# Optimization experiments

Hardware: AMD Instinct MI355X
Metric: run time of the kernel (lower is better)

The kernel has to match this reference:

```python
import jax, jax.numpy as jnp
import numpy as np

B, C, H, W, NH = 1, 192, 448, 448, 6
D = C // NH  # head dim = 32


def setup_inputs() -> dict:
    key = jax.random.key(0)
    ks = jax.random.split(key, 6)
    s = 0.02  # weight init scale
    return {
        "x": jax.random.normal(ks[0], (B, C, H, W), jnp.float32),
        "condition": jax.random.uniform(ks[1], (B, C, H, W), jnp.float32),
        "ln_g": jnp.ones((C,), jnp.float32),
        "ln_b": jnp.zeros((C,), jnp.float32),
        "pre_w": jax.random.normal(ks[2], (C, C), jnp.float32) * s,   # 1x1 conv [out,in]
        "pre_b": jnp.zeros((C,), jnp.float32),
        "qkv_w": jax.random.normal(ks[3], (3 * C, C), jnp.float32) * s,
        "mn_w": jax.random.normal(ks[4], (2 * D, D), jnp.float32) * s,  # Linear(d, 2d), [out,in]
        "gating": jnp.ones((1, 2 * NH, 1, 1), jnp.float32),
        "proj_w": jax.random.normal(ks[5], (C, C), jnp.float32) * s,
    }


def _gsa(x, condition, ln_g, ln_b, pre_w, pre_b, qkv_w, mn_w, gating, proj_w):
    b, c, h, w = x.shape
    nh = NH
    d = c // nh
    hw = h * w
    # ConvenientLayerNorm: LayerNorm over the channel axis per pixel (biased var, eps=1e-5)
    mu = jnp.mean(x, axis=1, keepdims=True)
    var = jnp.var(x, axis=1, keepdims=True)
    xn = (x - mu) * jax.lax.rsqrt(var + 1e-5)
    xn = xn * ln_g[None, :, None, None] + ln_b[None, :, None, None]
    # 1x1 convs == channel matmuls
    y = jnp.einsum('bchw,oc->bohw', xn, pre_w) + pre_b[None, :, None, None]
    qkv = jnp.einsum('bchw,oc->bohw', y, qkv_w)
    q, k, v = jnp.split(qkv, 3, axis=1)
    rs = lambda t: t.reshape(b, nh, d, hw)
    q, k, v = rs(q), rs(k), rs(v)
    # F.normalize over spatial axis (eps=1e-12)
    l2 = lambda t: t / jnp.maximum(jnp.linalg.norm(t, axis=-1, keepdims=True), 1e-12)
    q, k = l2(q), l2(k)
    # channel-wise attention scores [b,nh,d,d]
    attn = jnp.einsum('bhds,bhes->bhde', q, k)
    # mn_conv: Linear(d -> 2d) on last axis, then chunk
    mn = jnp.einsum('bhde,ge->bhdg', attn, mn_w)  # [b,nh,d,2d]
    m, n = jnp.split(mn, 2, axis=-1)
    g1, g2 = jnp.split(gating, 2, axis=1)  # each [1,nh,1,1]
    gm = g1 * m + g2 * n  # g1*(m@illu)+g2*(n@illu) == (g1*m+g2*n)@illu (per-head scalars)
    illu = condition.reshape(b, nh, d, hw)
    mi = jnp.einsum('bhde,bhes->bhds', gm, illu)  # [b,nh,d,hw]
    out = jax.nn.softmax(mi * v, axis=-2)  # softmax over head-dim axis d
    out = out.reshape(b, c, h, w)
    out = jnp.einsum('bchw,oc->bohw', out, proj_w) + x
    return out


def reference(x, condition, ln_g, ln_b, pre_w, pre_b, qkv_w, mn_w, gating, proj_w):
    return _gsa(x, condition, ln_g, ln_b, pre_w, pre_b, qkv_w, mn_w, gating, proj_w)
```

## Files before the change

### kernel.cpp

```cpp
#include <hip/hip_runtime.h>

typedef short s8v __attribute__((ext_vector_type(8)));
typedef short s4v __attribute__((ext_vector_type(4)));
typedef float f4v __attribute__((ext_vector_type(4)));

#define HW     200704
#define NCH    192
#define PT     64
#define CMP    68
#define PMP    200
#define GRID   512
#define NTILES 3136

__device__ __forceinline__ float b2f(unsigned short u){
    unsigned int i = ((unsigned int)u) << 16; float f;
    __builtin_memcpy(&f, &i, 4); return f;
}
__device__ __forceinline__ unsigned short f2b(float f){
    unsigned int i; __builtin_memcpy(&i, &f, 4);
    i += 0x7FFFu + ((i >> 16) & 1u);
    return (unsigned short)(i >> 16);
}
__device__ __forceinline__ int swz(int oct, int p){
    return (oct & ~7) | ((oct + 2*(p & 7)) & 7);
}

__global__ void gsa_prep(const float* __restrict__ pre_w, const float* __restrict__ qkv_w,
                         const float* __restrict__ proj_w, unsigned short* __restrict__ wbf,
                         float* __restrict__ accs, unsigned int* __restrict__ ctr)
{
    int i = blockIdx.x*256 + threadIdx.x;
    if (i < 2)      ctr[i] = 0u;
    if (i < 6528)   accs[i] = 0.f;
    if (i < 36864)  wbf[i]           = f2b(pre_w[i]);
    if (i < 110592) wbf[36864 + i]   = f2b(qkv_w[i]);
    if (i < 36864)  wbf[147456 + i]  = f2b(proj_w[i]);
}

__global__ __launch_bounds__(384, 3) void gsa_k1(
    const float* __restrict__ x,
    const float* __restrict__ lng,
    const float* __restrict__ lnb,
    const unsigned short* __restrict__ pre_wb,
    const float* __restrict__ pre_b,
    const unsigned short* __restrict__ qkv_wb,
    unsigned short* __restrict__ v_out,
    float* __restrict__ gram_red,
    float* __restrict__ sq_red,
    unsigned int* __restrict__ ctr)
{
    __shared__ __align__(16) unsigned char smem[26112*2 + 25600 + 1536];
    __shared__ int t_sh;
    unsigned short* bufA  = (unsigned short*)smem;
    unsigned short* bufP1 = (unsigned short*)(smem + 26112);
    unsigned short* bufP2 = (unsigned short*)(smem + 2*26112);
    float* sq_lds = (float*)(smem + 2*26112 + 25600);
    float* stats  = (float*)bufP2;

    const int tid  = threadIdx.x;
    const int wid  = tid >> 6;
    const int lane = tid & 63;
    const int l15  = lane & 15;
    const int quad = lane >> 4;

    f4v gacc[4];
    #pragma unroll
    for (int g = 0; g < 4; ++g) gacc[g] = (f4v){0.f, 0.f, 0.f, 0.f};
    sq_lds[tid] = 0.f;

    auto gemm2 = [&](int co, f4v (&acc)[2][4]) {
        #pragma unroll
        for (int j = 0; j < 2; ++j)
            #pragma unroll
            for (int nt = 0; nt < 4; ++nt) acc[j][nt] = (f4v){0.f,0.f,0.f,0.f};
        #pragma unroll
        for (int ks = 0; ks < 6; ++ks) {
            s8v a[2];
            #pragma unroll
            for (int j = 0; j < 2; ++j)
                a[j] = *(const s8v*)(qkv_wb + (size_t)(co*NCH + wid*32 + j*16 + l15)*NCH + ks*32 + quad*8);
            #pragma unroll
            for (int nt = 0; nt < 4; ++nt) {
                int p = nt*16 + l15;
                s8v b = *(const s8v*)(bufP2 + p*PMP + swz(ks*4 + quad, p)*8);
                #pragma unroll
                for (int j = 0; j < 2; ++j)
                    acc[j][nt] = __builtin_amdgcn_mfma_f32_16x16x32_bf16(a[j], b, acc[j][nt], 0, 0, 0);
            }
        }
    };

    for (;;) {
        __syncthreads();
        if (tid == 0) t_sh = atomicAdd(ctr, 1u);
        __syncthreads();
        const int t = t_sh;
        if (t >= NTILES) break;
        const int p0 = t * PT;

        {
            const int c0 = tid >> 3, oct = tid & 7;
            #pragma unroll
            for (int pass = 0; pass < 4; ++pass) {
                int c = pass*48 + c0;
                const float* gp = x + (size_t)c*HW + p0 + oct*8;
                f4v f0 = *(const f4v*)(gp);
                f4v f1 = *(const f4v*)(gp + 4);
                s8v w;
                #pragma unroll
                for (int r = 0; r < 4; ++r) { w[r] = (short)f2b(f0[r]); w[4+r] = (short)f2b(f1[r]); }
                *(s8v*)(bufA + c*CMP + oct*8) = w;
            }
        }
        __syncthreads();

        {
            const int p = lane, g = wid;
            float s1 = 0.f, s2 = 0.f;
            #pragma unroll
            for (int i = 0; i < 32; ++i) {
                float v = b2f(bufA[(g*32 + i)*CMP + p]);
                s1 += v; s2 += v*v;
            }
            stats[g*64 + p]       = s1;
            stats[384 + g*64 + p] = s2;
        }
        __syncthreads();
        if (tid < 64) {
            float s1 = 0.f, s2 = 0.f;
            #pragma unroll
            for (int g = 0; g < 6; ++g) { s1 += stats[g*64 + tid]; s2 += stats[384 + g*64 + tid]; }
            float mu  = s1 * (1.f/192.f);
            float var = s2 * (1.f/192.f) - mu*mu;
            stats[768 + tid] = mu;
            stats[832 + tid] = rsqrtf(fmaxf(var, 0.f) + 1e-5f);
        }
        __syncthreads();

        {
            const int p = lane, g = wid;
            const float mu = stats[768 + p], is = stats[832 + p];
            #pragma unroll
            for (int oo = 0; oo < 4; ++oo) {
                s8v w;
                #pragma unroll
                for (int j = 0; j < 8; ++j) {
                    int c = g*32 + oo*8 + j;
                    float v = (b2f(bufA[c*CMP + p]) - mu) * is;
                    v = v * lng[c] + lnb[c];
                    w[j] = (short)f2b(v);
                }
                int oct = g*4 + oo;
                *(s8v*)(bufP1 + p*PMP + swz(oct, p)*8) = w;
            }
        }
        __syncthreads();

        {
            f4v acc[2][4];
            #pragma unroll
            for (int j = 0; j < 2; ++j)
                #pragma unroll
                for (int nt = 0; nt < 4; ++nt) acc[j][nt] = (f4v){0.f,0.f,0.f,0.f};
            #pragma unroll
            for (int ks = 0; ks < 6; ++ks) {
                s8v a[2];
                #pragma unroll
                for (int j = 0; j < 2; ++j)
                    a[j] = *(const s8v*)(pre_wb + (size_t)((wid*2 + j)*16 + l15)*NCH + ks*32 + quad*8);
                #pragma unroll
                for (int nt = 0; nt < 4; ++nt) {
                    int p = nt*16 + l15;
                    s8v b = *(const s8v*)(bufP1 + p*PMP + swz(ks*4 + quad, p)*8);
                    #pragma unroll
                    for (int j = 0; j < 2; ++j)
                        acc[j][nt] = __builtin_amdgcn_mfma_f32_16x16x32_bf16(a[j], b, acc[j][nt], 0, 0, 0);
                }
            }
            #pragma unroll
            for (int j = 0; j < 2; ++j) {
                int c0 = (wid*2 + j)*16 + quad*4;
                f4v pb4 = *(const f4v*)(pre_b + c0);
                int oct = c0 >> 3, half = (c0 >> 2) & 1;
                #pragma unroll
                for (int nt = 0; nt < 4; ++nt) {
                    int p = nt*16 + l15;
                    s4v w;
                    #pragma unroll
                    for (int r = 0; r < 4; ++r)
                        w[r] = (short)f2b(acc[j][nt][r] + pb4[r]);
                    *(s4v*)(bufP2 + p*PMP + swz(oct, p)*8 + half*4) = w;
                }
            }
        }
        __syncthreads();

        {
            f4v acc[2][4];
            gemm2(0, acc);
            #pragma unroll
            for (int j = 0; j < 2; ++j)
                #pragma unroll
                for (int nt = 0; nt < 4; ++nt) {
                    int p = nt*16 + l15;
                    #pragma unroll
                    for (int r = 0; r < 4; ++r) {
                        int c = wid*32 + j*16 + quad*4 + r;
                        bufA[c*CMP + p] = f2b(acc[j][nt][r]);
                    }
                }
            gemm2(1, acc);
            #pragma unroll
            for (int j = 0; j < 2; ++j)
                #pragma unroll
                for (int nt = 0; nt < 4; ++nt) {
                    int p = nt*16 + l15;
                    #pragma unroll
                    for (int r = 0; r < 4; ++r) {
                        int c = wid*32 + j*16 + quad*4 + r;
                        bufP1[c*CMP + p] = f2b(acc[j][nt][r]);
                    }
                }
        }
        __syncthreads();

        {
            const unsigned short* src = (wid < 3) ? (bufA + tid*CMP) : (bufP1 + (tid - 192)*CMP);
            float s = 0.f;
            #pragma unroll
            for (int o = 0; o < 8; ++o) {
                s4v lo = *(const s4v*)(src + o*8);
                s4v hi = *(const s4v*)(src + o*8 + 4);
                #pragma unroll
                for (int e = 0; e < 4; ++e) {
                    float a = b2f((unsigned short)lo[e]);
                    float b = b2f((unsigned short)hi[e]);
                    s += a*a + b*b;
                }
            }
            sq_lds[tid] += s;
        }

        #pragma unroll
        for (int g = 0; g < 4; ++g) {
            int gt = wid*4 + g, h = gt >> 2, dm = (gt >> 1) & 1, em = gt & 1;
            const unsigned short* qrow = bufA  + (h*32 + dm*16 + l15)*CMP;
            const unsigned short* krow = bufP1 + (h*32 + em*16 + l15)*CMP;
            #pragma unroll
            for (int ks = 0; ks < 2; ++ks) {
                int off = ks*32 + quad*8;
                s4v alo = *(const s4v*)(qrow + off), ahi = *(const s4v*)(qrow + off + 4);
                s4v blo = *(const s4v*)(krow + off), bhi = *(const s4v*)(krow + off + 4);
                s8v a = __builtin_shufflevector(alo, ahi, 0,1,2,3,4,5,6,7);
                s8v b = __builtin_shufflevector(blo, bhi, 0,1,2,3,4,5,6,7);
                gacc[g] = __builtin_amdgcn_mfma_f32_16x16x32_bf16(a, b, gacc[g], 0, 0, 0);
            }
        }

        {
            f4v acc[2][4];
            gemm2(2, acc);
            __syncthreads();
            #pragma unroll
            for (int j = 0; j < 2; ++j)
                #pragma unroll
                for (int nt = 0; nt < 4; ++nt) {
                    int p = nt*16 + l15;
                    #pragma unroll
                    for (int r = 0; r < 4; ++r) {
                        int c = wid*32 + j*16 + quad*4 + r;
                        bufA[c*CMP + p] = f2b(acc[j][nt][r]);
                    }
                }
        }
        __syncthreads();
        {
            const int c0 = tid >> 3, oct = tid & 7;
            #pragma unroll
            for (int pass = 0; pass < 4; ++pass) {
                int c = pass*48 + c0;
                s4v lo = *(const s4v*)(bufA + c*CMP + oct*8);
                s4v hi = *(const s4v*)(bufA + c*CMP + oct*8 + 4);
                s8v w = __builtin_shufflevector(lo, hi, 0,1,2,3,4,5,6,7);
                *(s8v*)(v_out + 2*((size_t)c*HW + p0) + oct*8) = w;
            }
        }
    }

    #pragma unroll
    for (int g = 0; g < 4; ++g) {
        int gt = wid*4 + g, h = gt >> 2, dm = (gt >> 1) & 1, em = gt & 1;
        #pragma unroll
        for (int r = 0; r < 4; ++r) {
            int d = dm*16 + quad*4 + r, e = em*16 + l15;
            atomicAdd(&gram_red[h*1024 + d*32 + e], gacc[g][r]);
        }
    }
    atomicAdd(&sq_red[tid], sq_lds[tid]);
}

__global__ void gsa_k2(const float* __restrict__ gram_red, const float* __restrict__ sq_red,
                       const float* __restrict__ mn_w, const float* __restrict__ gating,
                       unsigned short* __restrict__ gm_out)
{
    __shared__ float attn[6144];
    __shared__ float mw[2048];
    __shared__ float inv[384];
    const int tid = threadIdx.x;
    for (int i = tid; i < 384; i += 256)
        inv[i] = 1.f / fmaxf(sqrtf(fmaxf(sq_red[i], 0.f)), 1e-12f);
    for (int i = tid; i < 2048; i += 256) mw[i] = mn_w[i];
    __syncthreads();
    for (int i = tid; i < 6144; i += 256) {
        int h = i >> 10, d = (i >> 5) & 31, e = i & 31;
        attn[i] = gram_red[i] * inv[h*32 + d] * inv[192 + h*32 + e];
    }
    __syncthreads();
    if (tid < 192) {
        int h = tid >> 5, d = tid & 31;
        float g1 = gating[h], g2 = gating[6 + h];
        const float* ar = attn + h*1024 + d*32;
        for (int e = 0; e < 32; ++e) {
            float m = 0.f, n = 0.f;
            for (int c2 = 0; c2 < 32; ++c2) {
                m += ar[c2] * mw[e*32 + c2];
                n += ar[c2] * mw[(e + 32)*32 + c2];
            }
            gm_out[h*1024 + d*32 + e] = f2b(g1*m + g2*n);
        }
    }
}

__global__ __launch_bounds__(384, 3) void gsa_k3(
    const float* __restrict__ cond,
    const float* __restrict__ x,
    const unsigned short* __restrict__ gm,
    const unsigned short* __restrict__ proj_wb,
    const unsigned short* v_in,
    float* out,
    unsigned int* __restrict__ ctr)
{
    __shared__ __align__(16) unsigned char smem[26112 + 25600 + 25600];
    __shared__ int t_sh;
    unsigned short* bufA = (unsigned short*)smem;
    unsigned short* bufB = (unsigned short*)(smem + 26112);
    unsigned short* bufC = (unsigned short*)(smem + 26112 + 25600);

    const int tid  = threadIdx.x;
    const int wid  = tid >> 6;
    const int lane = tid & 63;
    const int l15  = lane & 15;
    const int quad = lane >> 4;

    for (;;) {
        __syncthreads();
        if (tid == 0) t_sh = atomicAdd(ctr + 1, 1u);
        __syncthreads();
        const int t = t_sh;
        if (t >= NTILES) break;
        const int p0 = t * PT;

        {
            const int c0 = tid >> 3, oct = tid & 7;
            #pragma unroll
            for (int pass = 0; pass < 4; ++pass) {
                int c = pass*48 + c0;
                const float* gp = cond + (size_t)c*HW + p0 + oct*8;
                f4v f0 = *(const f4v*)(gp);
                f4v f1 = *(const f4v*)(gp + 4);
                s8v w;
                #pragma unroll
                for (int r = 0; r < 4; ++r) { w[r] = (short)f2b(f0[r]); w[4+r] = (short)f2b(f1[r]); }
                *(s8v*)(bufA + c*CMP + oct*8) = w;
            }
        }
        __syncthreads();
        {
            const int p = lane, g = wid;
            #pragma unroll
            for (int oo = 0; oo < 4; ++oo) {
                int oct = g*4 + oo;
                s8v w;
                #pragma unroll
                for (int j = 0; j < 8; ++j)
                    w[j] = (short)bufA[(oct*8 + j)*CMP + p];
                *(s8v*)(bufB + p*PMP + swz(oct, p)*8) = w;
            }
        }
        __syncthreads();
        {
            const int c0 = tid >> 3, oct = tid & 7;
            #pragma unroll
            for (int pass = 0; pass < 4; ++pass) {
                int c = pass*48 + c0;
                s8v vv = *(const s8v*)(v_in + 2*((size_t)c*HW + p0) + oct*8);
                s4v lo = __builtin_shufflevector(vv, vv, 0,1,2,3);
                s4v hi = __builtin_shufflevector(vv, vv, 4,5,6,7);
                *(s4v*)(bufA + c*CMP + oct*8)     = lo;
                *(s4v*)(bufA + c*CMP + oct*8 + 4) = hi;
            }
        }
        __syncthreads();

        {
            #pragma unroll
            for (int j = 0; j < 4; ++j) {
                int pr = wid*4 + j, h = pr >> 2, nt = pr & 3;
                int p = nt*16 + l15;
                s8v a0 = *(const s8v*)(gm + h*1024 + l15*32 + quad*8);
                s8v a1 = *(const s8v*)(gm + h*1024 + (16 + l15)*32 + quad*8);
                s8v b  = *(const s8v*)(bufB + p*PMP + swz(h*4 + quad, p)*8);
                f4v z = (f4v){0.f,0.f,0.f,0.f};
                f4v m0 = __builtin_amdgcn_mfma_f32_16x16x32_bf16(a0, b, z, 0, 0, 0);
                f4v m1 = __builtin_amdgcn_mfma_f32_16x16x32_bf16(a1, b, z, 0, 0, 0);
                float tv[8];
                #pragma unroll
                for (int r = 0; r < 4; ++r) {
                    tv[r]     = m0[r] * b2f(bufA[(h*32 + quad*4 + r)*CMP + p]);
                    tv[4 + r] = m1[r] * b2f(bufA[(h*32 + 16 + quad*4 + r)*CMP + p]);
                }
                float mx = tv[0];
                #pragma unroll
                for (int r = 1; r < 8; ++r) mx = fmaxf(mx, tv[r]);
                mx = fmaxf(mx, __shfl_xor(mx, 16));
                mx = fmaxf(mx, __shfl_xor(mx, 32));
                float s = 0.f;
                #pragma unroll
                for (int r = 0; r < 8; ++r) { tv[r] = __expf(tv[r] - mx); s += tv[r]; }
                s += __shfl_xor(s, 16);
                s += __shfl_xor(s, 32);
                float is = 1.f / s;
                s4v w0, w1;
                #pragma unroll
                for (int r = 0; r < 4; ++r) {
                    w0[r] = (short)f2b(tv[r] * is);
                    w1[r] = (short)f2b(tv[4 + r] * is);
                }
                int c0 = h*32 + quad*4, c1 = c0 + 16;
                *(s4v*)(bufC + p*PMP + swz(c0 >> 3, p)*8 + ((c0 >> 2) & 1)*4) = w0;
                *(s4v*)(bufC + p*PMP + swz(c1 >> 3, p)*8 + ((c1 >> 2) & 1)*4) = w1;
            }
        }
        __syncthreads();

        {
            f4v acc[2][4];
            #pragma unroll
            for (int j = 0; j < 2; ++j)
                #pragma unroll
                for (int nt = 0; nt < 4; ++nt) acc[j][nt] = (f4v){0.f,0.f,0.f,0.f};
            #pragma unroll
            for (int ks = 0; ks < 6; ++ks) {
                s8v a[2];
                #pragma unroll
                for (int j = 0; j < 2; ++j)
                    a[j] = *(const s8v*)(proj_wb + (size_t)((wid*2 + j)*16 + l15)*NCH + ks*32 + quad*8);
                #pragma unroll
                for (int nt = 0; nt < 4; ++nt) {
                    int p = nt*16 + l15;
                    s8v b = *(const s8v*)(bufC + p*PMP + swz(ks*4 + quad, p)*8);
                    #pragma unroll
                    for (int j = 0; j < 2; ++j)
                        acc[j][nt] = __builtin_amdgcn_mfma_f32_16x16x32_bf16(a[j], b, acc[j][nt], 0, 0, 0);
                }
            }
            __syncthreads();
            #pragma unroll
            for (int j = 0; j < 2; ++j)
                #pragma unroll
                for (int nt = 0; nt < 4; ++nt) {
                    int p = nt*16 + l15;
                    #pragma unroll
                    for (int r = 0; r < 4; ++r) {
                        int c = wid*32 + j*16 + quad*4 + r;
                        bufA[c*CMP + p] = f2b(acc[j][nt][r]);
                    }
                }
        }
        __syncthreads();

        {
            const int c0 = tid >> 3, oct = tid & 7;
            #pragma unroll
            for (int pass = 0; pass < 4; ++pass) {
                int c = pass*48 + c0;
                const float* xp = x + (size_t)c*HW + p0 + oct*8;
                f4v x0 = *(const f4v*)(xp);
                f4v x1 = *(const f4v*)(xp + 4);
                f4v o0, o1;
                #pragma unroll
                for (int r = 0; r < 4; ++r) {
                    o0[r] = b2f(bufA[c*CMP + oct*8 + r])     + x0[r];
                    o1[r] = b2f(bufA[c*CMP + oct*8 + 4 + r]) + x1[r];
                }
                float* op = out + (size_t)c*HW + p0 + oct*8;
                *(f4v*)(op)     = o0;
                *(f4v*)(op + 4) = o1;
            }
        }
    }
}

extern "C" void kernel_launch(void* const* d_in, const int* in_sizes, int n_in,
                              void* d_out, int out_size, void* d_ws, size_t ws_size,
                              hipStream_t stream)
{
    (void)in_sizes; (void)n_in; (void)out_size; (void)ws_size;
    const float* x      = (const float*)d_in[0];
    const float* cond   = (const float*)d_in[1];
    const float* lng    = (const float*)d_in[2];
    const float* lnb    = (const float*)d_in[3];
    const float* pre_w  = (const float*)d_in[4];
    const float* pre_b  = (const float*)d_in[5];
    const float* qkv_w  = (const float*)d_in[6];
    const float* mn_w   = (const float*)d_in[7];
    const float* gating = (const float*)d_in[8];
    const float* proj_w = (const float*)d_in[9];

    char* ws = (char*)d_ws;
    float* gram_red = (float*)ws;
    float* sq_red   = (float*)(ws + 24576);
    unsigned short* gm  = (unsigned short*)(ws + 26112);
    unsigned short* wbf = (unsigned short*)(ws + 38400);
    unsigned int* ctr   = (unsigned int*)(ws + 407040);
    unsigned short* pre_wb  = wbf;
    unsigned short* qkv_wb  = wbf + 36864;
    unsigned short* proj_wb = wbf + 147456;

    gsa_prep<<<432,  256, 0, stream>>>(pre_w, qkv_w, proj_w, wbf, gram_red, ctr);
    gsa_k1 <<<GRID,  384, 0, stream>>>(x, lng, lnb, pre_wb, pre_b, qkv_wb,
                                       (unsigned short*)d_out, gram_red, sq_red, ctr);
    gsa_k2 <<<1,     256, 0, stream>>>(gram_red, sq_red, mn_w, gating, gm);
    gsa_k3 <<<GRID,  384, 0, stream>>>(cond, x, gm, proj_wb,
                                       (const unsigned short*)d_out, (float*)d_out, ctr);
}
```

Baseline: 676.2 us.

## Prefetch next tile into registers and fuse QKV GEMMs into one pass

Both persistent kernels now take their first tile from blockIdx and prefetch the next tile's global inputs (x, or condition plus v) into registers while the current tile is being computed. Tile-counter atomics are issued early and the counters start at GRID. LayerNorm statistics are reduced with LDS atomics, which removes a sync and a serial reduction step. The three QKV GEMMs are merged into one pass that reuses the B fragments, and v is stored in a pixel-major layout so it can be copied directly. The costs are higher register pressure at 3 waves per SIMD and possible LDS atomic contention.

```diff
diff --git a/kernel.cpp b/kernel.cpp
--- a/kernel.cpp
+++ b/kernel.cpp
@@ -30,12 +30,13 @@
                          float* __restrict__ accs, unsigned int* __restrict__ ctr)
 {
     int i = blockIdx.x*256 + threadIdx.x;
-    if (i < 2)      ctr[i] = 0u;
+    if (i == 0) { ctr[0] = GRID; ctr[1] = GRID; }
     if (i < 6528)   accs[i] = 0.f;
     if (i < 36864)  wbf[i]           = f2b(pre_w[i]);
     if (i < 110592) wbf[36864 + i]   = f2b(qkv_w[i]);
     if (i < 36864)  wbf[147456 + i]  = f2b(proj_w[i]);
 }
+
 
 __global__ __launch_bounds__(384, 3) void gsa_k1(
     const float* __restrict__ x,
@@ -49,109 +50,75 @@
     float* __restrict__ sq_red,
     unsigned int* __restrict__ ctr)
 {
-    __shared__ __align__(16) unsigned char smem[26112*2 + 25600 + 1536];
-    __shared__ int t_sh;
+    __shared__ __align__(16) unsigned char smem[26112*2 + 25600 + 512 + 1536];
+    __shared__ int t_next_sh;
     unsigned short* bufA  = (unsigned short*)smem;
     unsigned short* bufP1 = (unsigned short*)(smem + 26112);
     unsigned short* bufP2 = (unsigned short*)(smem + 2*26112);
-    float* sq_lds = (float*)(smem + 2*26112 + 25600);
-    float* stats  = (float*)bufP2;
+    float* stats  = (float*)(smem + 2*26112 + 25600);
+    float* sq_lds = (float*)(smem + 2*26112 + 25600 + 512);
 
     const int tid  = threadIdx.x;
     const int wid  = tid >> 6;
     const int lane = tid & 63;
     const int l15  = lane & 15;
     const int quad = lane >> 4;
+    const int c0   = tid >> 3;
+    const int oc8  = tid & 7;
 
     f4v gacc[4];
     #pragma unroll
     for (int g = 0; g < 4; ++g) gacc[g] = (f4v){0.f, 0.f, 0.f, 0.f};
     sq_lds[tid] = 0.f;
 
-    auto gemm2 = [&](int co, f4v (&acc)[2][4]) {
-        #pragma unroll
-        for (int j = 0; j < 2; ++j)
-            #pragma unroll
-            for (int nt = 0; nt < 4; ++nt) acc[j][nt] = (f4v){0.f,0.f,0.f,0.f};
-        #pragma unroll
-        for (int ks = 0; ks < 6; ++ks) {
-            s8v a[2];
-            #pragma unroll
-            for (int j = 0; j < 2; ++j)
-                a[j] = *(const s8v*)(qkv_wb + (size_t)(co*NCH + wid*32 + j*16 + l15)*NCH + ks*32 + quad*8);
-            #pragma unroll
-            for (int nt = 0; nt < 4; ++nt) {
-                int p = nt*16 + l15;
-                s8v b = *(const s8v*)(bufP2 + p*PMP + swz(ks*4 + quad, p)*8);
-                #pragma unroll
-                for (int j = 0; j < 2; ++j)
-                    acc[j][nt] = __builtin_amdgcn_mfma_f32_16x16x32_bf16(a[j], b, acc[j][nt], 0, 0, 0);
-            }
-        }
-    };
-
-    for (;;) {
-        __syncthreads();
-        if (tid == 0) t_sh = atomicAdd(ctr, 1u);
-        __syncthreads();
-        const int t = t_sh;
-        if (t >= NTILES) break;
-        const int p0 = t * PT;
-
-        {
-            const int c0 = tid >> 3, oct = tid & 7;
-            #pragma unroll
-            for (int pass = 0; pass < 4; ++pass) {
-                int c = pass*48 + c0;
-                const float* gp = x + (size_t)c*HW + p0 + oct*8;
-                f4v f0 = *(const f4v*)(gp);
-                f4v f1 = *(const f4v*)(gp + 4);
-                s8v w;
-                #pragma unroll
-                for (int r = 0; r < 4; ++r) { w[r] = (short)f2b(f0[r]); w[4+r] = (short)f2b(f1[r]); }
-                *(s8v*)(bufA + c*CMP + oct*8) = w;
-            }
-        }
-        __syncthreads();
-
-        {
-            const int p = lane, g = wid;
+    int t = blockIdx.x;
+    f4v xr[8];
+    #pragma unroll
+    for (int pass = 0; pass < 4; ++pass) {
+        const float* gp = x + (size_t)(pass*48 + c0)*HW + t*PT + oc8*8;
+        xr[2*pass]   = *(const f4v*)(gp);
+        xr[2*pass+1] = *(const f4v*)(gp + 4);
+    }
+
+    while (t < NTILES) {
+        if (tid == 0) t_next_sh = (int)atomicAdd(ctr, 1u);
+        if (tid < 128) stats[tid] = 0.f;
+        #pragma unroll
+        for (int pass = 0; pass < 4; ++pass) {
+            int c = pass*48 + c0;
+            s8v w;
+            #pragma unroll
+            for (int r = 0; r < 4; ++r) { w[r] = (short)f2b(xr[2*pass][r]); w[4+r] = (short)f2b(xr[2*pass+1][r]); }
+            *(s8v*)(bufA + c*CMP + oc8*8) = w;
+        }
+        __syncthreads();
+
+        {
             float s1 = 0.f, s2 = 0.f;
             #pragma unroll
             for (int i = 0; i < 32; ++i) {
-                float v = b2f(bufA[(g*32 + i)*CMP + p]);
+                float v = b2f(bufA[(wid*32 + i)*CMP + lane]);
                 s1 += v; s2 += v*v;
             }
-            stats[g*64 + p]       = s1;
-            stats[384 + g*64 + p] = s2;
-        }
-        __syncthreads();
-        if (tid < 64) {
-            float s1 = 0.f, s2 = 0.f;
-            #pragma unroll
-            for (int g = 0; g < 6; ++g) { s1 += stats[g*64 + tid]; s2 += stats[384 + g*64 + tid]; }
-            float mu  = s1 * (1.f/192.f);
-            float var = s2 * (1.f/192.f) - mu*mu;
-            stats[768 + tid] = mu;
-            stats[832 + tid] = rsqrtf(fmaxf(var, 0.f) + 1e-5f);
-        }
-        __syncthreads();
-
-        {
-            const int p = lane, g = wid;
-            const float mu = stats[768 + p], is = stats[832 + p];
+            atomicAdd(&stats[lane], s1);
+            atomicAdd(&stats[64 + lane], s2);
+        }
+        __syncthreads();
+
+        {
+            const float mu = stats[lane] * (1.f/192.f);
+            const float is = rsqrtf(fmaxf(stats[64 + lane]*(1.f/192.f) - mu*mu, 0.f) + 1e-5f);
             #pragma unroll
             for (int oo = 0; oo < 4; ++oo) {
                 s8v w;
                 #pragma unroll
                 for (int j = 0; j < 8; ++j) {
-                    int c = g*32 + oo*8 + j;
-                    float v = (b2f(bufA[c*CMP + p]) - mu) * is;
+                    int c = wid*32 + oo*8 + j;
+                    float v = (b2f(bufA[c*CMP + lane]) - mu) * is;
                     v = v * lng[c] + lnb[c];
                     w[j] = (short)f2b(v);
                 }
-                int oct = g*4 + oo;
-                *(s8v*)(bufP1 + p*PMP + swz(oct, p)*8) = w;
+                *(s8v*)(bufP1 + lane*PMP + swz(wid*4 + oo, lane)*8) = w;
             }
         }
         __syncthreads();
@@ -164,24 +131,25 @@
                 for (int nt = 0; nt < 4; ++nt) acc[j][nt] = (f4v){0.f,0.f,0.f,0.f};
             #pragma unroll
             for (int ks = 0; ks < 6; ++ks) {
-                s8v a[2];
-                #pragma unroll
-                for (int j = 0; j < 2; ++j)
-                    a[j] = *(const s8v*)(pre_wb + (size_t)((wid*2 + j)*16 + l15)*NCH + ks*32 + quad*8);
+                s8v b[4];
                 #pragma unroll
                 for (int nt = 0; nt < 4; ++nt) {
                     int p = nt*16 + l15;
-                    s8v b = *(const s8v*)(bufP1 + p*PMP + swz(ks*4 + quad, p)*8);
+                    b[nt] = *(const s8v*)(bufP1 + p*PMP + swz(ks*4 + quad, p)*8);
+                }
+                #pragma unroll
+                for (int j = 0; j < 2; ++j) {
+                    s8v a = *(const s8v*)(pre_wb + (size_t)((wid*2 + j)*16 + l15)*NCH + ks*32 + quad*8);
                     #pragma unroll
-                    for (int j = 0; j < 2; ++j)
-                        acc[j][nt] = __builtin_amdgcn_mfma_f32_16x16x32_bf16(a[j], b, acc[j][nt], 0, 0, 0);
+                    for (int nt = 0; nt < 4; ++nt)
+                        acc[j][nt] = __builtin_amdgcn_mfma_f32_16x16x32_bf16(a, b[nt], acc[j][nt], 0, 0, 0);
                 }
             }
             #pragma unroll
             for (int j = 0; j < 2; ++j) {
-                int c0 = (wid*2 + j)*16 + quad*4;
-                f4v pb4 = *(const f4v*)(pre_b + c0);
-                int oct = c0 >> 3, half = (c0 >> 2) & 1;
+                int cc = (wid*2 + j)*16 + quad*4;
+                f4v pb4 = *(const f4v*)(pre_b + cc);
+                int oct = cc >> 3, half = (cc >> 2) & 1;
                 #pragma unroll
                 for (int nt = 0; nt < 4; ++nt) {
                     int p = nt*16 + l15;
@@ -195,9 +163,39 @@
         }
         __syncthreads();
 
-        {
-            f4v acc[2][4];
-            gemm2(0, acc);
+        f4v av[2][4];
+        {
+            f4v aq[2][4], ak[2][4];
+            #pragma unroll
+            for (int j = 0; j < 2; ++j)
+                #pragma unroll
+                for (int nt = 0; nt < 4; ++nt) {
+                    aq[j][nt] = (f4v){0.f,0.f,0.f,0.f};
+                    ak[j][nt] = (f4v){0.f,0.f,0.f,0.f};
+                    av[j][nt] = (f4v){0.f,0.f,0.f,0.f};
+                }
+            #pragma unroll
+            for (int ks = 0; ks < 6; ++ks) {
+                s8v b[4];
+                #pragma unroll
+                for (int nt = 0; nt < 4; ++nt) {
+                    int p = nt*16 + l15;
+                    b[nt] = *(const s8v*)(bufP2 + p*PMP + swz(ks*4 + quad, p)*8);
+                }
+                #pragma unroll
+                for (int j = 0; j < 2; ++j) {
+                    const unsigned short* wr = qkv_wb + (size_t)(wid*32 + j*16 + l15)*NCH + ks*32 + quad*8;
+                    s8v a0 = *(const s8v*)(wr);
+                    s8v a1 = *(const s8v*)(wr + (size_t)192*NCH);
+                    s8v a2 = *(const s8v*)(wr + (size_t)384*NCH);
+                    #pragma unroll
+                    for (int nt = 0; nt < 4; ++nt) {
+                        aq[j][nt] = __builtin_amdgcn_mfma_f32_16x16x32_bf16(a0, b[nt], aq[j][nt], 0, 0, 0);
+                        ak[j][nt] = __builtin_amdgcn_mfma_f32_16x16x32_bf16(a1, b[nt], ak[j][nt], 0, 0, 0);
+                        av[j][nt] = __builtin_amdgcn_mfma_f32_16x16x32_bf16(a2, b[nt], av[j][nt], 0, 0, 0);
+                    }
+                }
+            }
             #pragma unroll
             for (int j = 0; j < 2; ++j)
                 #pragma unroll
@@ -206,26 +204,38 @@
                     #pragma unroll
                     for (int r = 0; r < 4; ++r) {
                         int c = wid*32 + j*16 + quad*4 + r;
-                        bufA[c*CMP + p] = f2b(acc[j][nt][r]);
+                        bufA[c*CMP + p]  = f2b(aq[j][nt][r]);
+                        bufP1[c*CMP + p] = f2b(ak[j][nt][r]);
                     }
                 }
-            gemm2(1, acc);
-            #pragma unroll
-            for (int j = 0; j < 2; ++j)
-                #pragma unroll
-                for (int nt = 0; nt < 4; ++nt) {
-                    int p = nt*16 + l15;
-                    #pragma unroll
-                    for (int r = 0; r < 4; ++r) {
-                        int c = wid*32 + j*16 + quad*4 + r;
-                        bufP1[c*CMP + p] = f2b(acc[j][nt][r]);
-                    }
-                }
-        }
-        __syncthreads();
-
-        {
-            const unsigned short* src = (wid < 3) ? (bufA + tid*CMP) : (bufP1 + (tid - 192)*CMP);
+        }
+        __syncthreads();
+
+        int tn = t_next_sh;
+        if (tn < NTILES) {
+            #pragma unroll
+            for (int pass = 0; pass < 4; ++pass) {
+                const float* gp = x + (size_t)(pass*48 + c0)*HW + tn*PT + oc8*8;
+                xr[2*pass]   = *(const f4v*)(gp);
+                xr[2*pass+1] = *(const f4v*)(gp + 4);
+            }
+        }
+        #pragma unroll
+        for (int j = 0; j < 2; ++j) {
+            int cc = wid*32 + j*16 + quad*4;
+            int oct = cc >> 3, half = (cc >> 2) & 1;
+            #pragma unroll
+            for (int nt = 0; nt < 4; ++nt) {
+                int p = nt*16 + l15;
+                s4v w;
+                #pragma unroll
+                for (int r = 0; r < 4; ++r)
+                    w[r] = (short)f2b(av[j][nt][r]);
+                *(s4v*)(bufP2 + p*PMP + swz(oct, p)*8 + half*4) = w;
+            }
+        }
+        {
+            const unsigned short* src = (tid < 192) ? (bufA + tid*CMP) : (bufP1 + (tid - 192)*CMP);
             float s = 0.f;
             #pragma unroll
             for (int o = 0; o < 8; ++o) {
@@ -240,12 +250,11 @@
             }
             sq_lds[tid] += s;
         }
-
         #pragma unroll
         for (int g = 0; g < 4; ++g) {
-            int gt = wid*4 + g, h = gt >> 2, dm = (gt >> 1) & 1, em = gt & 1;
-            const unsigned short* qrow = bufA  + (h*32 + dm*16 + l15)*CMP;
-            const unsigned short* krow = bufP1 + (h*32 + em*16 + l15)*CMP;
+            int dm = g >> 1, em = g & 1;
+            const unsigned short* qrow = bufA  + (wid*32 + dm*16 + l15)*CMP;
+            const unsigned short* krow = bufP1 + (wid*32 + em*16 + l15)*CMP;
             #pragma unroll
             for (int ks = 0; ks < 2; ++ks) {
                 int off = ks*32 + quad*8;
@@ -256,44 +265,26 @@
                 gacc[g] = __builtin_amdgcn_mfma_f32_16x16x32_bf16(a, b, gacc[g], 0, 0, 0);
             }
         }
-
-        {
-            f4v acc[2][4];
-            gemm2(2, acc);
-            __syncthreads();
-            #pragma unroll
-            for (int j = 0; j < 2; ++j)
-                #pragma unroll
-                for (int nt = 0; nt < 4; ++nt) {
-                    int p = nt*16 + l15;
-                    #pragma unroll
-                    for (int r = 0; r < 4; ++r) {
-                        int c = wid*32 + j*16 + quad*4 + r;
-                        bufA[c*CMP + p] = f2b(acc[j][nt][r]);
-                    }
-                }
-        }
-        __syncthreads();
-        {
-            const int c0 = tid >> 3, oct = tid & 7;
-            #pragma unroll
-            for (int pass = 0; pass < 4; ++pass) {
-                int c = pass*48 + c0;
-                s4v lo = *(const s4v*)(bufA + c*CMP + oct*8);
-                s4v hi = *(const s4v*)(bufA + c*CMP + oct*8 + 4);
-                s8v w = __builtin_shufflevector(lo, hi, 0,1,2,3,4,5,6,7);
-                *(s8v*)(v_out + 2*((size_t)c*HW + p0) + oct*8) = w;
-            }
-        }
+        __syncthreads();
+
+        #pragma unroll
+        for (int q = 0; q < 4; ++q) {
+            int idx = q*384 + tid;
+            int p   = idx / 24;
+            int col = (idx - p*24) * 8;
+            s8v w = *(const s8v*)(bufP2 + p*PMP + col);
+            *(s8v*)(v_out + (size_t)4*(idx >> 4)*HW + (size_t)128*t + (tid & 15)*8) = w;
+        }
+        t = tn;
     }
 
     #pragma unroll
     for (int g = 0; g < 4; ++g) {
-        int gt = wid*4 + g, h = gt >> 2, dm = (gt >> 1) & 1, em = gt & 1;
+        int dm = g >> 1, em = g & 1;
         #pragma unroll
         for (int r = 0; r < 4; ++r) {
             int d = dm*16 + quad*4 + r, e = em*16 + l15;
-            atomicAdd(&gram_red[h*1024 + d*32 + e], gacc[g][r]);
+            atomicAdd(&gram_red[wid*1024 + d*32 + e], gacc[g][r]);
         }
     }
     atomicAdd(&sq_red[tid], sq_lds[tid]);
@@ -341,7 +332,7 @@
     unsigned int* __restrict__ ctr)
 {
     __shared__ __align__(16) unsigned char smem[26112 + 25600 + 25600];
-    __shared__ int t_sh;
+    __shared__ int t_next_sh;
     unsigned short* bufA = (unsigned short*)smem;
     unsigned short* bufB = (unsigned short*)(smem + 26112);
     unsigned short* bufC = (unsigned short*)(smem + 26112 + 25600);
@@ -351,73 +342,87 @@
     const int lane = tid & 63;
     const int l15  = lane & 15;
     const int quad = lane >> 4;
-
-    for (;;) {
-        __syncthreads();
-        if (tid == 0) t_sh = atomicAdd(ctr + 1, 1u);
-        __syncthreads();
-        const int t = t_sh;
-        if (t >= NTILES) break;
-        const int p0 = t * PT;
-
-        {
-            const int c0 = tid >> 3, oct = tid & 7;
+    const int c0   = tid >> 3;
+    const int oc8  = tid & 7;
+
+    int t = blockIdx.x;
+    f4v cr[8];
+    s8v vr[4];
+    #pragma unroll
+    for (int pass = 0; pass < 4; ++pass) {
+        const float* gp = cond + (size_t)(pass*48 + c0)*HW + t*PT + oc8*8;
+        cr[2*pass]   = *(const f4v*)(gp);
+        cr[2*pass+1] = *(const f4v*)(gp + 4);
+    }
+    #pragma unroll
+    for (int q = 0; q < 4; ++q) {
+        int idx = q*384 + tid;
+        vr[q] = *(const s8v*)(v_in + (size_t)4*(idx >> 4)*HW + (size_t)128*t + (tid & 15)*8);
+    }
+
+    while (t < NTILES) {
+        __syncthreads();
+        if (tid == 0) t_next_sh = (int)atomicAdd(ctr + 1, 1u);
+        #pragma unroll
+        for (int pass = 0; pass < 4; ++pass) {
+            int c = pass*48 + c0;
+            s8v w;
+            #pragma unroll
+            for (int r = 0; r < 4; ++r) { w[r] = (short)f2b(cr[2*pass][r]); w[4+r] = (short)f2b(cr[2*pass+1][r]); }
+            *(s8v*)(bufA + c*CMP + oc8*8) = w;
+        }
+        __syncthreads();
+        #pragma unroll
+        for (int oo = 0; oo < 4; ++oo) {
+            int oct = wid*4 + oo;
+            s8v w;
+            #pragma unroll
+            for (int j = 0; j < 8; ++j)
+                w[j] = (short)bufA[(oct*8 + j)*CMP + lane];
+            *(s8v*)(bufB + lane*PMP + swz(oct, lane)*8) = w;
+        }
+        __syncthreads();
+        #pragma unroll
+        for (int q = 0; q < 4; ++q) {
+            int idx = q*384 + tid;
+            int p   = idx / 24;
+            int col = (idx - p*24) * 8;
+            *(s8v*)(bufA + p*PMP + col) = vr[q];
+        }
+        int tn = t_next_sh;
+        if (tn < NTILES) {
             #pragma unroll
             for (int pass = 0; pass < 4; ++pass) {
-                int c = pass*48 + c0;
-                const float* gp = cond + (size_t)c*HW + p0 + oct*8;
-                f4v f0 = *(const f4v*)(gp);
-                f4v f1 = *(const f4v*)(gp + 4);
-                s8v w;
-                #pragma unroll
-                for (int r = 0; r < 4; ++r) { w[r] = (short)f2b(f0[r]); w[4+r] = (short)f2b(f1[r]); }
-                *(s8v*)(bufA + c*CMP + oct*8) = w;
-            }
-        }
-        __syncthreads();
-        {
-            const int p = lane, g = wid;
-            #pragma unroll
-            for (int oo = 0; oo < 4; ++oo) {
-                int oct = g*4 + oo;
-                s8v w;
-                #pragma unroll
-                for (int j = 0; j < 8; ++j)
-                    w[j] = (short)bufA[(oct*8 + j)*CMP + p];
-                *(s8v*)(bufB + p*PMP + swz(oct, p)*8) = w;
-            }
-        }
-        __syncthreads();
-        {
-            const int c0 = tid >> 3, oct = tid & 7;
-            #pragma unroll
-            for (int pass = 0; pass < 4; ++pass) {
-                int c = pass*48 + c0;
-                s8v vv = *(const s8v*)(v_in + 2*((size_t)c*HW + p0) + oct*8);
-                s4v lo = __builtin_shufflevector(vv, vv, 0,1,2,3);
-                s4v hi = __builtin_shufflevector(vv, vv, 4,5,6,7);
-                *(s4v*)(bufA + c*CMP + oct*8)     = lo;
-                *(s4v*)(bufA + c*CMP + oct*8 + 4) = hi;
-            }
-        }
-        __syncthreads();
-
-        {
-            #pragma unroll
-            for (int j = 0; j < 4; ++j) {
-                int pr = wid*4 + j, h = pr >> 2, nt = pr & 3;
+                const float* gp = cond + (size_t)(pass*48 + c0)*HW + tn*PT + oc8*8;
+                cr[2*pass]   = *(const f4v*)(gp);
+                cr[2*pass+1] = *(const f4v*)(gp + 4);
+            }
+            #pragma unroll
+            for (int q = 0; q < 4; ++q) {
+                int idx = q*384 + tid;
+                vr[q] = *(const s8v*)(v_in + (size_t)4*(idx >> 4)*HW + (size_t)128*tn + (tid & 15)*8);
+            }
+        }
+        __syncthreads();
+        {
+            const int h = wid;
+            s8v a0 = *(const s8v*)(gm + h*1024 + l15*32 + quad*8);
+            s8v a1 = *(const s8v*)(gm + h*1024 + (16 + l15)*32 + quad*8);
+            #pragma unroll
+            for (int nt = 0; nt < 4; ++nt) {
                 int p = nt*16 + l15;
-                s8v a0 = *(const s8v*)(gm + h*1024 + l15*32 + quad*8);
-                s8v a1 = *(const s8v*)(gm + h*1024 + (16 + l15)*32 + quad*8);
-                s8v b  = *(const s8v*)(bufB + p*PMP + swz(h*4 + quad, p)*8);
+                s8v b = *(const s8v*)(bufB + p*PMP + swz(h*4 + quad, p)*8);
                 f4v z = (f4v){0.f,0.f,0.f,0.f};
                 f4v m0 = __builtin_amdgcn_mfma_f32_16x16x32_bf16(a0, b, z, 0, 0, 0);
                 f4v m1 = __builtin_amdgcn_mfma_f32_16x16x32_bf16(a1, b, z, 0, 0, 0);
+                int oct0 = h*4 + (quad >> 1), hf = (quad & 1)*4;
+                s4v v0 = *(const s4v*)(bufA + p*PMP + swz(oct0, p)*8 + hf);
+                s4v v1 = *(const s4v*)(bufA + p*PMP + swz(oct0 + 2, p)*8 + hf);
                 float tv[8];
                 #pragma unroll
                 for (int r = 0; r < 4; ++r) {
-                    tv[r]     = m0[r] * b2f(bufA[(h*32 + quad*4 + r)*CMP + p]);
-                    tv[4 + r] = m1[r] * b2f(bufA[(h*32 + 16 + quad*4 + r)*CMP + p]);
+                    tv[r]     = m0[r] * b2f((unsigned short)v0[r]);
+                    tv[4 + r] = m1[r] * b2f((unsigned short)v1[r]);
                 }
                 float mx = tv[0];
                 #pragma unroll
@@ -436,14 +441,20 @@
                     w0[r] = (short)f2b(tv[r] * is);
                     w1[r] = (short)f2b(tv[4 + r] * is);
                 }
-                int c0 = h*32 + quad*4, c1 = c0 + 16;
-                *(s4v*)(bufC + p*PMP + swz(c0 >> 3, p)*8 + ((c0 >> 2) & 1)*4) = w0;
-                *(s4v*)(bufC + p*PMP + swz(c1 >> 3, p)*8 + ((c1 >> 2) & 1)*4) = w1;
-            }
-        }
-        __syncthreads();
-
-        {
+                int ca = h*32 + quad*4, cb = ca + 16;
+                *(s4v*)(bufC + p*PMP + swz(ca >> 3, p)*8 + ((ca >> 2) & 1)*4) = w0;
+                *(s4v*)(bufC + p*PMP + swz(cb >> 3, p)*8 + ((cb >> 2) & 1)*4) = w1;
+            }
+        }
+        __syncthreads();
+        {
+            f4v xr[8];
+            #pragma unroll
+            for (int pass = 0; pass < 4; ++pass) {
+                const float* gp = x + (size_t)(pass*48 + c0)*HW + t*PT + oc8*8;
+                xr[2*pass]   = *(const f4v*)(gp);
+                xr[2*pass+1] = *(const f4v*)(gp + 4);
+            }
             f4v acc[2][4];
             #pragma unroll
             for (int j = 0; j < 2; ++j)
@@ -451,20 +462,20 @@
                 for (int nt = 0; nt < 4; ++nt) acc[j][nt] = (f4v){0.f,0.f,0.f,0.f};
             #pragma unroll
             for (int ks = 0; ks < 6; ++ks) {
-                s8v a[2];
-                #pragma unroll
-                for (int j = 0; j < 2; ++j)
-                    a[j] = *(const s8v*)(proj_wb + (size_t)((wid*2 + j)*16 + l15)*NCH + ks*32 + quad*8);
+                s8v b[4];
                 #pragma unroll
                 for (int nt = 0; nt < 4; ++nt) {
                     int p = nt*16 + l15;
-                    s8v b = *(const s8v*)(bufC + p*PMP + swz(ks*4 + quad, p)*8);
+                    b[nt] = *(const s8v*)(bufC + p*PMP + swz(ks*4 + quad, p)*8);
+                }
+                #pragma unroll
+                for (int j = 0; j < 2; ++j) {
+                    s8v a = *(const s8v*)(proj_wb + (size_t)((wid*2 + j)*16 + l15)*NCH + ks*32 + quad*8);
                     #pragma unroll
-                    for (int j = 0; j < 2; ++j)
-                        acc[j][nt] = __builtin_amdgcn_mfma_f32_16x16x32_bf16(a[j], b, acc[j][nt], 0, 0, 0);
-                }
-            }
-            __syncthreads();
+                    for (int nt = 0; nt < 4; ++nt)
+                        acc[j][nt] = __builtin_amdgcn_mfma_f32_16x16x32_bf16(a, b[nt], acc[j][nt], 0, 0, 0);
+                }
+            }
             #pragma unroll
             for (int j = 0; j < 2; ++j)
                 #pragma unroll
@@ -476,28 +487,22 @@
                         bufA[c*CMP + p] = f2b(acc[j][nt][r]);
                     }
                 }
-        }
-        __syncthreads();
-
-        {
-            const int c0 = tid >> 3, oct = tid & 7;
+            __syncthreads();
             #pragma unroll
             for (int pass = 0; pass < 4; ++pass) {
                 int c = pass*48 + c0;
-                const float* xp = x + (size_t)c*HW + p0 + oct*8;
-                f4v x0 = *(const f4v*)(xp);
-                f4v x1 = *(const f4v*)(xp + 4);
                 f4v o0, o1;
                 #pragma unroll
                 for (int r = 0; r < 4; ++r) {
-                    o0[r] = b2f(bufA[c*CMP + oct*8 + r])     + x0[r];
-                    o1[r] = b2f(bufA[c*CMP + oct*8 + 4 + r]) + x1[r];
-                }
-                float* op = out + (size_t)c*HW + p0 + oct*8;
+                    o0[r] = b2f(bufA[c*CMP + oc8*8 + r])     + xr[2*pass][r];
+                    o1[r] = b2f(bufA[c*CMP + oc8*8 + 4 + r]) + xr[2*pass+1][r];
+                }
+                float* op = out + (size_t)c*HW + t*PT + oc8*8;
                 *(f4v*)(op)     = o0;
                 *(f4v*)(op + 4) = o1;
             }
         }
+        t = tn;
     }
 }
 
```

Measured after the change: 970.9 us. 1.44x slower.
